# Kernel tuning notes

Measured on AMD Instinct MI355X. Metric: run time of the kernel, lower is better.

Reference implementation:

```python
import jax, jax.numpy as jnp
import numpy as np

B, N, C = 1, 4096, 1024
H = 16
HD = C // H  # head_dim = 64
SCALE = HD ** -0.5


def setup_inputs() -> dict:
    key = jax.random.key(0)
    k1, k2, k3, k4, k5 = jax.random.split(key, 5)
    x1 = jax.random.normal(k1, (B, N, C), dtype=jnp.float32)
    x2 = jax.random.normal(k2, (B, N, C), dtype=jnp.float32)
    # qkv: Linear(dim, 2*all_head_dim), bias=False. Stored as (in, out) for x @ W.
    W_qkv = jax.random.normal(k3, (C, 2 * H * HD), dtype=jnp.float32) * (C ** -0.5)
    # proj: Linear(all_head_dim, dim) with bias
    W_proj = jax.random.normal(k4, (H * HD, C), dtype=jnp.float32) * ((H * HD) ** -0.5)
    b_proj = jax.random.normal(k5, (C,), dtype=jnp.float32) * 0.01
    return {"x1": x1, "x2": x2, "W_qkv": W_qkv, "W_proj": W_proj, "b_proj": b_proj}


def reference(x1, x2, W_qkv, W_proj, b_proj):
    b, n, c = x1.shape
    # qk projection: (B,N,2*H*HD) -> (2,B,H,N,HD)
    qkv = (x1 @ W_qkv).reshape(b, n, 2, H, HD).transpose(2, 0, 3, 1, 4)
    q, k = qkv[0], qkv[1]  # (B,H,N,HD)
    # V2: reshape (N,1,H,HD) then permute -> (1,H,N,HD); valid since B==1
    v = x2.reshape(n, 1, H, HD).transpose(1, 2, 0, 3)
    attn = jax.nn.softmax(jnp.einsum('bhnd,bhmd->bhnm', q * SCALE, k), axis=-1)
    out = jnp.einsum('bhnm,bhmd->bhnd', attn, v)  # broadcasts v over batch
    out = out.transpose(0, 2, 1, 3).reshape(b, n, H * HD)
    return out @ W_proj + b_proj
```

## Files before the change

kernel.cpp:

```cpp
#include <hip/hip_runtime.h>

typedef unsigned short u16;
typedef unsigned int u32;

#define HNUM 16
#define NSEQ 4096
#define CDIM 1024
#define SCALE 0.125f
#define LOG2E 1.4426950408889634f

using bf16x8 = __attribute__((ext_vector_type(8))) __bf16;
using f32x4  = __attribute__((ext_vector_type(4))) float;

__device__ __forceinline__ u16 f2bf(float f) {
  union { float f; u32 u; } v; v.f = f;
  u32 u = v.u;
  return (u16)((u + 0x7fffu + ((u >> 16) & 1u)) >> 16);
}
__device__ __forceinline__ float fexp2(float x) { return __builtin_amdgcn_exp2f(x); }

__device__ __forceinline__ f32x4 mfma16(bf16x8 a, bf16x8 b, f32x4 c) {
  return __builtin_amdgcn_mfma_f32_16x16x32_bf16(a, b, c, 0, 0, 0);
}

__device__ __forceinline__ bf16x8 pack8(f32x4 a, f32x4 b) {
  union { f32x4 v; u32 u[4]; } A, B;
  A.v = a; B.v = b;
  union { u32 u[4]; bf16x8 h; } R;
  R.u[0] = __builtin_amdgcn_perm(A.u[1] + 0x8000u, A.u[0] + 0x8000u, 0x07060302u);
  R.u[1] = __builtin_amdgcn_perm(A.u[3] + 0x8000u, A.u[2] + 0x8000u, 0x07060302u);
  R.u[2] = __builtin_amdgcn_perm(B.u[1] + 0x8000u, B.u[0] + 0x8000u, 0x07060302u);
  R.u[3] = __builtin_amdgcn_perm(B.u[3] + 0x8000u, B.u[2] + 0x8000u, 0x07060302u);
  return R.h;
}

template <int ROWS>
__device__ __forceinline__ void stage64(const u16* __restrict__ g, int ldg,
                                        u16* __restrict__ lds, int tid) {
#pragma unroll
  for (int i = 0; i < ROWS * 8 / 256; ++i) {
    const int cid = i * 256 + tid;
    const int r = cid >> 3, c8 = (cid & 7) * 8;
    *(bf16x8*)(lds + r * 64 + c8) = *(const bf16x8*)(g + r * ldg + c8);
  }
}

template <int ROWS>
__device__ __forceinline__ void stage64f(const float* __restrict__ g, int ldg,
                                         u16* __restrict__ lds, int tid) {
#pragma unroll
  for (int i = 0; i < ROWS * 8 / 256; ++i) {
    const int cid = i * 256 + tid;
    const int r = cid >> 3, c8 = (cid & 7) * 8;
    const float4 f0 = *(const float4*)(g + r * ldg + c8);
    const float4 f1 = *(const float4*)(g + r * ldg + c8 + 4);
    u16 tmp[8] = {f2bf(f0.x), f2bf(f0.y), f2bf(f0.z), f2bf(f0.w),
                  f2bf(f1.x), f2bf(f1.y), f2bf(f1.z), f2bf(f1.w)};
    *(bf16x8*)(lds + r * 64 + c8) = *(bf16x8*)tmp;
  }
}

__global__ __launch_bounds__(256) void cvtT_k(const float* __restrict__ in,
                                              u16* __restrict__ out, int R, int C,
                                              int scaleRows, float scale) {
  __shared__ u16 t[64][65];
  const int tid = threadIdx.x;
  const int r0 = blockIdx.y * 64, c0 = blockIdx.x * 64;
  const int tr = tid >> 2, tc = (tid & 3) * 16;
  const float s = (c0 < scaleRows) ? scale : 1.0f;
  const float* src = in + (r0 + tr) * C + c0 + tc;
#pragma unroll
  for (int i = 0; i < 16; ++i) t[tr][tc + i] = f2bf(src[i] * s);
  __syncthreads();
  u16* dst = out + (c0 + tr) * R + r0 + tc;
#pragma unroll
  for (int i = 0; i < 16; ++i) dst[i] = t[tc + i][tr];
}

__global__ __launch_bounds__(256) void gemm1_k(const float* __restrict__ A,
                                               const u16* __restrict__ Bt,
                                               u16* __restrict__ C,
                                               int M, int N, int K) {
  __shared__ __align__(16) u16 As[128 * 64];
  __shared__ __align__(16) u16 Bs[128 * 64];
  const int tid = threadIdx.x;
  const int wave = tid >> 6, lane = tid & 63;
  const int quad = lane >> 4, l16 = lane & 15;
  const int m0 = blockIdx.y * 128, n0 = blockIdx.x * 128;
  const int wm = (wave >> 1) * 64, wn = (wave & 1) * 64;

  f32x4 acc[4][4] = {};
  for (int k0 = 0; k0 < K; k0 += 64) {
    stage64f<128>(A + m0 * K + k0, K, As, tid);
    stage64<128>(Bt + n0 * K + k0, K, Bs, tid);
    __syncthreads();
#pragma unroll
    for (int ks = 0; ks < 2; ++ks) {
      bf16x8 a[4], b[4];
#pragma unroll
      for (int mt = 0; mt < 4; ++mt)
        a[mt] = *(const bf16x8*)(As + (wm + mt * 16 + l16) * 64 + ks * 32 + quad * 8);
#pragma unroll
      for (int nt = 0; nt < 4; ++nt)
        b[nt] = *(const bf16x8*)(Bs + (wn + nt * 16 + l16) * 64 + ks * 32 + quad * 8);
#pragma unroll
      for (int mt = 0; mt < 4; ++mt)
#pragma unroll
        for (int nt = 0; nt < 4; ++nt)
          acc[mt][nt] = mfma16(a[mt], b[nt], acc[mt][nt]);
    }
    __syncthreads();
  }
#pragma unroll
  for (int mt = 0; mt < 4; ++mt)
#pragma unroll
    for (int nt = 0; nt < 4; ++nt)
#pragma unroll
      for (int r = 0; r < 4; ++r)
        C[(m0 + wm + mt * 16 + quad * 4 + r) * N + n0 + wn + nt * 16 + l16] =
            f2bf(acc[mt][nt][r]);
}

__global__ __launch_bounds__(256) void gemm2_k(const u16* __restrict__ A,
                                               const u16* __restrict__ Bt,
                                               float* __restrict__ C,
                                               const float* __restrict__ bias,
                                               int M, int N, int K) {
  __shared__ __align__(16) u16 As[128 * 64];
  __shared__ __align__(16) u16 Bs[128 * 64];
  const int tid = threadIdx.x;
  const int wave = tid >> 6, lane = tid & 63;
  const int quad = lane >> 4, l16 = lane & 15;
  const int m0 = blockIdx.y * 128, n0 = blockIdx.x * 128;
  const int wm = (wave >> 1) * 64, wn = (wave & 1) * 64;

  f32x4 acc[4][4] = {};
  for (int k0 = 0; k0 < K; k0 += 64) {
    stage64<128>(A + m0 * K + k0, K, As, tid);
    stage64<128>(Bt + n0 * K + k0, K, Bs, tid);
    __syncthreads();
#pragma unroll
    for (int ks = 0; ks < 2; ++ks) {
      bf16x8 a[4], b[4];
#pragma unroll
      for (int mt = 0; mt < 4; ++mt)
        a[mt] = *(const bf16x8*)(As + (wm + mt * 16 + l16) * 64 + ks * 32 + quad * 8);
#pragma unroll
      for (int nt = 0; nt < 4; ++nt)
        b[nt] = *(const bf16x8*)(Bs + (wn + nt * 16 + l16) * 64 + ks * 32 + quad * 8);
#pragma unroll
      for (int mt = 0; mt < 4; ++mt)
#pragma unroll
        for (int nt = 0; nt < 4; ++nt)
          acc[mt][nt] = mfma16(a[mt], b[nt], acc[mt][nt]);
    }
    __syncthreads();
  }
#pragma unroll
  for (int mt = 0; mt < 4; ++mt)
#pragma unroll
    for (int nt = 0; nt < 4; ++nt)
#pragma unroll
      for (int r = 0; r < 4; ++r) {
        const int col = n0 + wn + nt * 16 + l16;
        C[(m0 + wm + mt * 16 + quad * 4 + r) * N + col] = acc[mt][nt][r] + bias[col];
      }
}

#define KPAD 72
#define PPAD 68
__global__ __launch_bounds__(128) void attn_k(const u16* __restrict__ QK,
                                              const u16* __restrict__ Vt,
                                              u16* __restrict__ O) {
  __shared__ __align__(16) u16 Ks[64 * KPAD];
  __shared__ __align__(16) u16 Vs[64 * KPAD];
  __shared__ __align__(16) float Ps[2][32 * PPAD];
  const int tid = threadIdx.x;
  const int wave = tid >> 6, lane = tid & 63;
  const int quad = lane >> 4, l16 = lane & 15;
  const int head = blockIdx.y;
  const int qw = blockIdx.x * 64 + wave * 32;

  bf16x8 qf[2][2];
#pragma unroll
  for (int mt = 0; mt < 2; ++mt)
#pragma unroll
    for (int ks = 0; ks < 2; ++ks)
      qf[mt][ks] = *(const bf16x8*)(QK + (qw + mt * 16 + l16) * 2048 + head * 64 +
                                    ks * 32 + quad * 8);

  f32x4 o[2][4] = {};
  float lsum[8] = {};
  float* Pw = Ps[wave];

  for (int kt0 = 0; kt0 < NSEQ; kt0 += 64) {
#pragma unroll
    for (int c = 0; c < 4; ++c) {
      const int idx = c * 128 + tid;
      const int row = idx >> 3, c8 = (idx & 7) * 8;
      *(bf16x8*)(Ks + row * KPAD + c8) =
          *(const bf16x8*)(QK + (kt0 + row) * 2048 + CDIM + head * 64 + c8);
      *(bf16x8*)(Vs + row * KPAD + c8) =
          *(const bf16x8*)(Vt + (head * 64 + row) * NSEQ + kt0 + c8);
    }
    __syncthreads();

    f32x4 s[2][4] = {};
#pragma unroll
    for (int ks = 0; ks < 2; ++ks)
#pragma unroll
      for (int nt = 0; nt < 4; ++nt) {
        bf16x8 kf = *(const bf16x8*)(Ks + (nt * 16 + l16) * KPAD + ks * 32 + quad * 8);
#pragma unroll
        for (int mt = 0; mt < 2; ++mt)
          s[mt][nt] = mfma16(qf[mt][ks], kf, s[mt][nt]);
      }

#pragma unroll
    for (int mt = 0; mt < 2; ++mt)
#pragma unroll
      for (int nt = 0; nt < 4; ++nt)
#pragma unroll
        for (int r = 0; r < 4; ++r) {
          const float p = fexp2(s[mt][nt][r]);
          lsum[mt * 4 + r] += p;
          Pw[(mt * 16 + quad * 4 + r) * PPAD + nt * 16 + l16] = p;
        }

#pragma unroll
    for (int ks = 0; ks < 2; ++ks) {
      bf16x8 pf[2];
#pragma unroll
      for (int mt = 0; mt < 2; ++mt) {
        const float* pp = Pw + (mt * 16 + l16) * PPAD + ks * 32 + quad * 8;
        pf[mt] = pack8(*(const f32x4*)pp, *(const f32x4*)(pp + 4));
      }
#pragma unroll
      for (int nt = 0; nt < 4; ++nt) {
        bf16x8 vf = *(const bf16x8*)(Vs + (nt * 16 + l16) * KPAD + ks * 32 + quad * 8);
#pragma unroll
        for (int mt = 0; mt < 2; ++mt)
          o[mt][nt] = mfma16(pf[mt], vf, o[mt][nt]);
      }
    }
    __syncthreads();
  }

#pragma unroll
  for (int j = 0; j < 8; ++j) {
#pragma unroll
    for (int d = 1; d < 16; d <<= 1) lsum[j] += __shfl_xor(lsum[j], d, 64);
    lsum[j] = 1.0f / lsum[j];
  }
#pragma unroll
  for (int mt = 0; mt < 2; ++mt)
#pragma unroll
    for (int nt = 0; nt < 4; ++nt)
#pragma unroll
      for (int r = 0; r < 4; ++r)
        O[(qw + mt * 16 + quad * 4 + r) * CDIM + head * 64 + nt * 16 + l16] =
            f2bf(o[mt][nt][r] * lsum[mt * 4 + r]);
}

extern "C" void kernel_launch(void* const* d_in, const int* in_sizes, int n_in,
                              void* d_out, int out_size, void* d_ws, size_t ws_size,
                              hipStream_t stream) {
  const float* x1    = (const float*)d_in[0];
  const float* x2    = (const float*)d_in[1];
  const float* Wqkv  = (const float*)d_in[2];
  const float* Wproj = (const float*)d_in[3];
  const float* bproj = (const float*)d_in[4];
  float* out = (float*)d_out;

  char* ws = (char*)d_ws;
  u16* QK  = (u16*)(ws);
  u16* Vt  = (u16*)(ws + 16u * 1024 * 1024);
  u16* Obf = (u16*)(ws + 24u * 1024 * 1024);
  u16* WpT = (u16*)(ws + 32u * 1024 * 1024);
  u16* WqT = (u16*)(ws + 34u * 1024 * 1024);

  const float cfac = SCALE * LOG2E;

  cvtT_k<<<dim3(2048 / 64, 1024 / 64), 256, 0, stream>>>(Wqkv, WqT, 1024, 2048,
                                                         1024, cfac);
  cvtT_k<<<dim3(1024 / 64, 1024 / 64), 256, 0, stream>>>(Wproj, WpT, 1024, 1024,
                                                         0, 1.0f);
  cvtT_k<<<dim3(1024 / 64, 4096 / 64), 256, 0, stream>>>(x2, Vt, 4096, 1024,
                                                         0, 1.0f);

  gemm1_k<<<dim3(2048 / 128, 4096 / 128), 256, 0, stream>>>(x1, WqT, QK,
                                                            4096, 2048, 1024);
  attn_k<<<dim3(4096 / 64, HNUM), 128, 0, stream>>>(QK, Vt, Obf);
  gemm2_k<<<dim3(1024 / 128, 4096 / 128), 256, 0, stream>>>(Obf, WpT, out, bproj,
                                                            4096, 1024, 1024);
}
```

Baseline: 278.4 us.

## Enlarge attention query tile, store P as swizzled bf16, use direct global-to-LDS loads

The attention kernel now handles 64 query rows per wave instead of 32, halving the number of K/V tile loads per query row. It computes S transposed (K as the A operand) so each lane can pack exp2 results straight into bf16 P tiles in LDS using an XOR swizzle, replacing the padded fp32 P buffer and its repacking. K/V tiles, and the bf16 operands of both GEMMs, are loaded with global_load_lds directly into XOR-swizzled or unpadded LDS, bypassing registers. The trade-offs are a halved attention grid (fewer blocks to fill the CUs), higher register pressure from the larger accumulators, and a more intricate swizzle and row-sum shuffle scheme.

```diff
diff --git a/kernel.cpp b/kernel.cpp
--- a/kernel.cpp
+++ b/kernel.cpp
@@ -23,26 +23,17 @@
   return __builtin_amdgcn_mfma_f32_16x16x32_bf16(a, b, c, 0, 0, 0);
 }
 
-__device__ __forceinline__ bf16x8 pack8(f32x4 a, f32x4 b) {
-  union { f32x4 v; u32 u[4]; } A, B;
-  A.v = a; B.v = b;
-  union { u32 u[4]; bf16x8 h; } R;
-  R.u[0] = __builtin_amdgcn_perm(A.u[1] + 0x8000u, A.u[0] + 0x8000u, 0x07060302u);
-  R.u[1] = __builtin_amdgcn_perm(A.u[3] + 0x8000u, A.u[2] + 0x8000u, 0x07060302u);
-  R.u[2] = __builtin_amdgcn_perm(B.u[1] + 0x8000u, B.u[0] + 0x8000u, 0x07060302u);
-  R.u[3] = __builtin_amdgcn_perm(B.u[3] + 0x8000u, B.u[2] + 0x8000u, 0x07060302u);
-  return R.h;
-}
-
-template <int ROWS>
-__device__ __forceinline__ void stage64(const u16* __restrict__ g, int ldg,
-                                        u16* __restrict__ lds, int tid) {
-#pragma unroll
-  for (int i = 0; i < ROWS * 8 / 256; ++i) {
-    const int cid = i * 256 + tid;
-    const int r = cid >> 3, c8 = (cid & 7) * 8;
-    *(bf16x8*)(lds + r * 64 + c8) = *(const bf16x8*)(g + r * ldg + c8);
-  }
+__device__ __forceinline__ u32 pack2(float a, float b) {
+  union { float f; u32 u; } A, B;
+  A.f = a; B.f = b;
+  return __builtin_amdgcn_perm(B.u + 0x8000u, A.u + 0x8000u, 0x07060302u);
+}
+
+__device__ __forceinline__ void g2l16(const void* g, void* l) {
+  __builtin_amdgcn_global_load_lds(
+      (const __attribute__((address_space(1))) unsigned int*)(unsigned long long)g,
+      (__attribute__((address_space(3))) unsigned int*)(unsigned int)(unsigned long long)l,
+      16, 0, 0);
 }
 
 template <int ROWS>
@@ -88,11 +79,16 @@
   const int quad = lane >> 4, l16 = lane & 15;
   const int m0 = blockIdx.y * 128, n0 = blockIdx.x * 128;
   const int wm = (wave >> 1) * 64, wn = (wave & 1) * 64;
+  const int lrow = lane >> 3, lc8 = (lane & 7) * 8;
 
   f32x4 acc[4][4] = {};
   for (int k0 = 0; k0 < K; k0 += 64) {
+#pragma unroll
+    for (int c = 0; c < 4; ++c) {
+      const int cw = wave * 4 + c;
+      g2l16(Bt + (n0 + cw * 8 + lrow) * K + k0 + lc8, (char*)Bs + cw * 1024);
+    }
     stage64f<128>(A + m0 * K + k0, K, As, tid);
-    stage64<128>(Bt + n0 * K + k0, K, Bs, tid);
     __syncthreads();
 #pragma unroll
     for (int ks = 0; ks < 2; ++ks) {
@@ -133,11 +129,16 @@
   const int quad = lane >> 4, l16 = lane & 15;
   const int m0 = blockIdx.y * 128, n0 = blockIdx.x * 128;
   const int wm = (wave >> 1) * 64, wn = (wave & 1) * 64;
+  const int lrow = lane >> 3, lc8 = (lane & 7) * 8;
 
   f32x4 acc[4][4] = {};
   for (int k0 = 0; k0 < K; k0 += 64) {
-    stage64<128>(A + m0 * K + k0, K, As, tid);
-    stage64<128>(Bt + n0 * K + k0, K, Bs, tid);
+#pragma unroll
+    for (int c = 0; c < 4; ++c) {
+      const int cw = wave * 4 + c;
+      g2l16(A  + (m0 + cw * 8 + lrow) * K + k0 + lc8, (char*)As + cw * 1024);
+      g2l16(Bt + (n0 + cw * 8 + lrow) * K + k0 + lc8, (char*)Bs + cw * 1024);
+    }
     __syncthreads();
 #pragma unroll
     for (int ks = 0; ks < 2; ++ks) {
@@ -167,99 +168,106 @@
       }
 }
 
-#define KPAD 72
-#define PPAD 68
 __global__ __launch_bounds__(128) void attn_k(const u16* __restrict__ QK,
                                               const u16* __restrict__ Vt,
                                               u16* __restrict__ O) {
-  __shared__ __align__(16) u16 Ks[64 * KPAD];
-  __shared__ __align__(16) u16 Vs[64 * KPAD];
-  __shared__ __align__(16) float Ps[2][32 * PPAD];
+  __shared__ __align__(16) u16 Ks[64 * 64];
+  __shared__ __align__(16) u16 Vs[64 * 64];
+  __shared__ __align__(16) u16 Ps[2][64 * 64];
   const int tid = threadIdx.x;
   const int wave = tid >> 6, lane = tid & 63;
   const int quad = lane >> 4, l16 = lane & 15;
   const int head = blockIdx.y;
-  const int qw = blockIdx.x * 64 + wave * 32;
-
-  bf16x8 qf[2][2];
-#pragma unroll
-  for (int mt = 0; mt < 2; ++mt)
+  const int qb = blockIdx.x * 128 + wave * 64;
+  const int lrow = lane >> 3;
+  const int lc8 = ((lane & 7) ^ lrow) * 8;
+  const int swz = ((quad ^ (l16 & 7))) * 8;
+
+  bf16x8 qf[4][2];
+#pragma unroll
+  for (int mt = 0; mt < 4; ++mt)
 #pragma unroll
     for (int ks = 0; ks < 2; ++ks)
-      qf[mt][ks] = *(const bf16x8*)(QK + (qw + mt * 16 + l16) * 2048 + head * 64 +
+      qf[mt][ks] = *(const bf16x8*)(QK + (qb + mt * 16 + l16) * 2048 + head * 64 +
                                     ks * 32 + quad * 8);
 
-  f32x4 o[2][4] = {};
-  float lsum[8] = {};
-  float* Pw = Ps[wave];
+  f32x4 o[4][4] = {};
+  float lsum[4] = {};
+  u16* Pw = Ps[wave];
 
   for (int kt0 = 0; kt0 < NSEQ; kt0 += 64) {
 #pragma unroll
     for (int c = 0; c < 4; ++c) {
-      const int idx = c * 128 + tid;
-      const int row = idx >> 3, c8 = (idx & 7) * 8;
-      *(bf16x8*)(Ks + row * KPAD + c8) =
-          *(const bf16x8*)(QK + (kt0 + row) * 2048 + CDIM + head * 64 + c8);
-      *(bf16x8*)(Vs + row * KPAD + c8) =
-          *(const bf16x8*)(Vt + (head * 64 + row) * NSEQ + kt0 + c8);
-    }
-    __syncthreads();
-
-    f32x4 s[2][4] = {};
+      const int cw = wave * 4 + c;
+      const int row = cw * 8 + lrow;
+      g2l16(QK + (kt0 + row) * 2048 + CDIM + head * 64 + lc8, (char*)Ks + cw * 1024);
+      g2l16(Vt + (head * 64 + row) * NSEQ + kt0 + lc8,        (char*)Vs + cw * 1024);
+    }
+    __syncthreads();
+
+    f32x4 s[4][4] = {};
 #pragma unroll
     for (int ks = 0; ks < 2; ++ks)
 #pragma unroll
       for (int nt = 0; nt < 4; ++nt) {
-        bf16x8 kf = *(const bf16x8*)(Ks + (nt * 16 + l16) * KPAD + ks * 32 + quad * 8);
-#pragma unroll
-        for (int mt = 0; mt < 2; ++mt)
-          s[mt][nt] = mfma16(qf[mt][ks], kf, s[mt][nt]);
+        const bf16x8 kf =
+            *(const bf16x8*)(Ks + (nt * 16 + l16) * 64 + (swz ^ (ks * 32)));
+#pragma unroll
+        for (int mt = 0; mt < 4; ++mt)
+          s[mt][nt] = mfma16(kf, qf[mt][ks], s[mt][nt]);
       }
 
 #pragma unroll
-    for (int mt = 0; mt < 2; ++mt)
-#pragma unroll
-      for (int nt = 0; nt < 4; ++nt)
-#pragma unroll
-        for (int r = 0; r < 4; ++r) {
-          const float p = fexp2(s[mt][nt][r]);
-          lsum[mt * 4 + r] += p;
-          Pw[(mt * 16 + quad * 4 + r) * PPAD + nt * 16 + l16] = p;
-        }
+    for (int mt = 0; mt < 4; ++mt)
+#pragma unroll
+      for (int nt = 0; nt < 4; ++nt) {
+        const float p0 = fexp2(s[mt][nt][0]);
+        const float p1 = fexp2(s[mt][nt][1]);
+        const float p2 = fexp2(s[mt][nt][2]);
+        const float p3 = fexp2(s[mt][nt][3]);
+        lsum[mt] += (p0 + p1) + (p2 + p3);
+        u32 d01 = pack2(p0, p1), d23 = pack2(p2, p3);
+        const int col8 = (nt * 2 + (quad >> 1)) ^ (l16 & 7);
+        u32* dst = (u32*)(Pw + (mt * 16 + l16) * 64 + col8 * 8 + (quad & 1) * 4);
+        dst[0] = d01; dst[1] = d23;
+      }
 
 #pragma unroll
     for (int ks = 0; ks < 2; ++ks) {
-      bf16x8 pf[2];
-#pragma unroll
-      for (int mt = 0; mt < 2; ++mt) {
-        const float* pp = Pw + (mt * 16 + l16) * PPAD + ks * 32 + quad * 8;
-        pf[mt] = pack8(*(const f32x4*)pp, *(const f32x4*)(pp + 4));
+      bf16x8 pf[4];
+#pragma unroll
+      for (int mt = 0; mt < 4; ++mt)
+        pf[mt] = *(const bf16x8*)(Pw + (mt * 16 + l16) * 64 + (swz ^ (ks * 32)));
+#pragma unroll
+      for (int dt = 0; dt < 4; ++dt) {
+        const bf16x8 vf =
+            *(const bf16x8*)(Vs + (dt * 16 + l16) * 64 + (swz ^ (ks * 32)));
+#pragma unroll
+        for (int mt = 0; mt < 4; ++mt)
+          o[mt][dt] = mfma16(pf[mt], vf, o[mt][dt]);
       }
-#pragma unroll
-      for (int nt = 0; nt < 4; ++nt) {
-        bf16x8 vf = *(const bf16x8*)(Vs + (nt * 16 + l16) * KPAD + ks * 32 + quad * 8);
-#pragma unroll
-        for (int mt = 0; mt < 2; ++mt)
-          o[mt][nt] = mfma16(pf[mt], vf, o[mt][nt]);
-      }
-    }
-    __syncthreads();
-  }
-
-#pragma unroll
-  for (int j = 0; j < 8; ++j) {
-#pragma unroll
-    for (int d = 1; d < 16; d <<= 1) lsum[j] += __shfl_xor(lsum[j], d, 64);
-    lsum[j] = 1.0f / lsum[j];
-  }
-#pragma unroll
-  for (int mt = 0; mt < 2; ++mt)
-#pragma unroll
-    for (int nt = 0; nt < 4; ++nt)
-#pragma unroll
-      for (int r = 0; r < 4; ++r)
-        O[(qw + mt * 16 + quad * 4 + r) * CDIM + head * 64 + nt * 16 + l16] =
-            f2bf(o[mt][nt][r] * lsum[mt * 4 + r]);
+    }
+    __syncthreads();
+  }
+
+  float linv[4];
+#pragma unroll
+  for (int mt = 0; mt < 4; ++mt) {
+    float v = lsum[mt];
+    v += __shfl_xor(v, 16, 64);
+    v += __shfl_xor(v, 32, 64);
+    linv[mt] = 1.0f / v;
+  }
+#pragma unroll
+  for (int mt = 0; mt < 4; ++mt)
+#pragma unroll
+    for (int r = 0; r < 4; ++r) {
+      const float lv = __shfl(linv[mt], (lane & 48) | (quad * 4 + r), 64);
+#pragma unroll
+      for (int dt = 0; dt < 4; ++dt)
+        O[(qb + mt * 16 + quad * 4 + r) * CDIM + head * 64 + dt * 16 + l16] =
+            f2bf(o[mt][dt][r] * lv);
+    }
 }
 
 extern "C" void kernel_launch(void* const* d_in, const int* in_sizes, int n_in,
@@ -290,7 +298,7 @@
 
   gemm1_k<<<dim3(2048 / 128, 4096 / 128), 256, 0, stream>>>(x1, WqT, QK,
                                                             4096, 2048, 1024);
-  attn_k<<<dim3(4096 / 64, HNUM), 128, 0, stream>>>(QK, Vt, Obf);
+  attn_k<<<dim3(4096 / 128, HNUM), 128, 0, stream>>>(QK, Vt, Obf);
   gemm2_k<<<dim3(1024 / 128, 4096 / 128), 256, 0, stream>>>(Obf, WpT, out, bproj,
                                                             4096, 1024, 1024);
 }
```

Result: slower. 292.5 us (+5.1%).
